# Optimization experiments

Hardware: AMD Instinct MI355X
Metric: run time of the kernel (lower is better)

## Reference

```python
import jax, jax.numpy as jnp
import numpy as np

N, S, D = 4, 2048, 1024
H, HD = 16, 64  # heads, head_dim = patch_size // heads
SCALE = 1.0 / np.float32(np.sqrt(D))  # module divides by sqrt(patch_size), not sqrt(head_dim)


def setup_inputs() -> dict:
    key = jax.random.key(0)
    ks = jax.random.split(key, 8)
    return {
        "values": jax.random.normal(ks[0], (N, S, D), dtype=jnp.float32),
        "keys": jax.random.normal(ks[1], (N, S, D), dtype=jnp.float32),
        "query": jax.random.normal(ks[2], (N, S, D), dtype=jnp.float32),
        "Wv": jax.random.normal(ks[3], (HD, HD), dtype=jnp.float32) / np.float32(np.sqrt(HD)),
        "Wk": jax.random.normal(ks[4], (HD, HD), dtype=jnp.float32) / np.float32(np.sqrt(HD)),
        "Wq": jax.random.normal(ks[5], (HD, HD), dtype=jnp.float32) / np.float32(np.sqrt(HD)),
        "Wo": jax.random.normal(ks[6], (D, D), dtype=jnp.float32) / np.float32(np.sqrt(D)),
        "bo": jnp.zeros((D,), dtype=jnp.float32),
    }


def reference(values, keys, query, Wv, Wk, Wq, Wo, bo):
    n, ql = query.shape[0], query.shape[1]
    # reshape to heads, then per-head shared linear projections (torch Linear: x @ W.T)
    v = jnp.einsum('nlhd,ed->nlhe', values.reshape(n, -1, H, HD), Wv)
    k = jnp.einsum('nkhd,ed->nkhe', keys.reshape(n, -1, H, HD), Wk)
    q = jnp.einsum('nqhd,ed->nqhe', query.reshape(n, -1, H, HD), Wq)
    energy = jnp.einsum('nqhd,nkhd->nhqk', q, k)  # [N,H,Sq,Sk]
    attn = jax.nn.softmax(energy * SCALE, axis=3)
    out = jnp.einsum('nhql,nlhd->nqhd', attn, v).reshape(n, ql, H * HD)
    return out @ Wo.T + bo
```

## Files before the change

### kernel.cpp

```cpp
#include <hip/hip_runtime.h>
#include <stdint.h>

typedef _Float16 f16;
typedef f16 half2_t __attribute__((ext_vector_type(2)));
typedef f16 half4_t __attribute__((ext_vector_type(4)));
typedef f16 half8_t __attribute__((ext_vector_type(8)));
typedef __fp16 fp16x2_t __attribute__((ext_vector_type(2)));
typedef float f32x4 __attribute__((ext_vector_type(4)));

#define N_ 4
#define S_ 2048
#define D_ 1024
#define H_ 16
#define HD_ 64
#define LOG2E 1.44269504088896340736f
#define SCALE_ 0.03125f

typedef __attribute__((address_space(1))) void gvoid;
typedef __attribute__((address_space(3))) void lvoid;

__device__ __forceinline__ void load_lds16(const void* g, void* l) {
  __builtin_amdgcn_global_load_lds((gvoid*)(uintptr_t)g, (lvoid*)l, 16, 0, 0);
}

__device__ __forceinline__ f32x4 mfma32(half8_t a, half8_t b, f32x4 c) {
  return __builtin_amdgcn_mfma_f32_16x16x32_f16(a, b, c, 0, 0, 0);
}

__device__ __forceinline__ half2_t pack_f16(float a, float b) {
  fp16x2_t t = __builtin_amdgcn_cvt_pkrtz(a, b);
  return __builtin_bit_cast(half2_t, t);
}

__global__ void wprep(const float* __restrict__ Wv, const float* __restrict__ Wo,
                      const float* __restrict__ Wq, const float* __restrict__ Wk,
                      const float* __restrict__ V,
                      f16* __restrict__ Wbig, float* __restrict__ Mq,
                      f16* __restrict__ v16) {
  __shared__ char smem[16384];
  int b = blockIdx.x;
  if (b < 1024) {
    int j = b;
#pragma unroll
    for (int c = 0; c < 4; ++c) {
      int i = c * 256 + threadIdx.x;
      int h = i >> 6, dd = i & 63;
      const float* wo = Wo + (size_t)j * 1024 + h * 64;
      float acc = 0.f;
#pragma unroll 8
      for (int e = 0; e < 64; ++e) acc += Wv[e * 64 + dd] * wo[e];
      Wbig[(size_t)j * 1024 + i] = (f16)acc;
    }
  } else if (b < 1040) {
    int tid = (b - 1024) * 256 + threadIdx.x;
    int d = tid >> 6, e = tid & 63;
    float acc = 0.f;
#pragma unroll 8
    for (int r = 0; r < 64; ++r) acc += Wq[r * 64 + d] * Wk[r * 64 + e];
    Mq[d * 64 + e] = acc * (SCALE_ * LOG2E);
  } else {
    f16* lv = (f16*)smem;
    int b2 = b - 1040;
    int n = b2 >> 10, hh = (b2 >> 6) & 15, sb = b2 & 63;
    int t = threadIdx.x;
    {
      int r = t >> 3, ic = t & 7;
      const float* src = V + ((size_t)(n * S_ + sb * 32 + r)) * D_ + hh * HD_ + ic * 8;
      f32x4 a = *(const f32x4*)src;
      f32x4 b3 = *(const f32x4*)(src + 4);
      half8_t hv;
#pragma unroll
      for (int j = 0; j < 4; ++j) { hv[j] = (f16)a[j]; hv[4 + j] = (f16)b3[j]; }
      *(half8_t*)(lv + r * 64 + ic * 8) = hv;
    }
    __syncthreads();
    {
      int mt = t >> 6, L = t & 63;
      int quad = L >> 4, ld = L & 15;
      half8_t o;
#pragma unroll
      for (int j = 0; j < 4; ++j) {
        o[j]     = lv[(quad * 4 + j) * 64 + mt * 16 + ld];
        o[4 + j] = lv[(quad * 4 + j + 16) * 64 + mt * 16 + ld];
      }
      *(half8_t*)(v16 + (((size_t)(n * 16 + hh) * 64 + sb) * 4 + mt) * 512 + L * 8) = o;
    }
  }
}

__global__ __launch_bounds__(256, 3) void prep_qk(const float* __restrict__ Q,
                                                  const float* __restrict__ K,
                                                  const float* __restrict__ Mq,
                                                  f16* __restrict__ q16,
                                                  f16* __restrict__ k16) {
  __shared__ char smem[49152];
  int b = blockIdx.x;
  int hhalf = b & 1;
  int sblk = (b >> 1) & 127;
  int n = b >> 8;
  int t = threadIdx.x;
  int L = t & 63, w = t >> 6;

  const char* Qblk = (const char*)(Q + ((size_t)(n * S_ + sblk * 16)) * D_) + hhalf * 2048;
#pragma unroll
  for (int i = 0; i < 8; ++i) {
    int g = (w * 8 + i) * 64 + L;
    int row = g >> 7, hhg = (g >> 4) & 7, sl = g & 15;
    load_lds16(Qblk + (size_t)row * 4096 + hhg * 256 + ((sl ^ (row & 7)) << 4),
               smem + (w * 8 + i) * 1024);
  }
#pragma unroll
  for (int j = 0; j < 4; ++j)
    load_lds16((const char*)Mq + (size_t)(((w * 4 + j) * 64 + L) << 4),
               smem + 32768 + (w * 4 + j) * 1024);

  const char* Kblk = (const char*)(K + ((size_t)(n * S_ + sblk * 16)) * D_) + hhalf * 2048;
#pragma unroll
  for (int i = 0; i < 4; ++i) {
    int e = i * 256 + t;
    int r = e >> 6, c6 = e & 63;
    const char* src = Kblk + (size_t)r * 4096 + c6 * 32;
    f32x4 a = *(const f32x4*)src;
    f32x4 b2 = *(const f32x4*)(src + 16);
    half8_t hv;
#pragma unroll
    for (int jj = 0; jj < 4; ++jj) { hv[jj] = (f16)a[jj]; hv[4 + jj] = (f16)b2[jj]; }
    int hk = hhalf * 8 + (c6 >> 3), cc = c6 & 7, dp = cc >> 2, qd = cc & 3;
    *(half8_t*)(k16 + ((((size_t)(n * 16 + hk) * 128 + sblk) * 2 + dp) * 512) +
                (qd * 16 + r) * 8) = hv;
  }
  __syncthreads();

  int lq = t & 15, hh8 = (t >> 4) & 7, eh = t >> 7;
  int head = hhalf * 8 + hh8;
  const float* mql = (const float*)(smem + 32768);
  f32x4 acc4[8];
#pragma unroll
  for (int i = 0; i < 8; ++i) acc4[i] = (f32x4){0.f, 0.f, 0.f, 0.f};
  for (int d4 = 0; d4 < 16; ++d4) {
    f32x4 qv = *(const f32x4*)(smem + lq * 2048 + hh8 * 256 + ((d4 ^ (lq & 7)) << 4));
#pragma unroll
    for (int dj = 0; dj < 4; ++dj) {
      const f32x4* mrow = (const f32x4*)(mql + (d4 * 4 + dj) * 64 + eh * 32);
      float qs = qv[dj];
#pragma unroll
      for (int i = 0; i < 8; ++i) acc4[i] += mrow[i] * qs;
    }
  }
  size_t cbase = ((size_t)((n * 16 + head) * 128 + sblk)) * 2;
#pragma unroll
  for (int qd = 0; qd < 4; ++qd) {
    half8_t hv;
    f32x4 a0 = acc4[qd * 2], a1 = acc4[qd * 2 + 1];
#pragma unroll
    for (int jj = 0; jj < 4; ++jj) { hv[jj] = (f16)a0[jj]; hv[4 + jj] = (f16)a1[jj]; }
    *(half8_t*)(q16 + (cbase + eh) * 512 + (qd * 16 + lq) * 8) = hv;
  }
}

__global__ __launch_bounds__(256, 2) void flash(const f16* __restrict__ q16,
                                                const f16* __restrict__ k16,
                                                const f16* __restrict__ v16,
                                                f16* __restrict__ att) {
  int nh = blockIdx.x;
  int qt = blockIdx.y;
  int L = threadIdx.x & 63, w = threadIdx.x >> 6;
  int lq = L & 15, quad = L >> 4;

  const half8_t* qg = (const half8_t*)q16;
  half8_t qB[4][2];
#pragma unroll
  for (int j = 0; j < 4; ++j) {
    size_t qc = ((size_t)(nh * 128 + qt * 16 + w * 4 + j)) * 2;
    qB[j][0] = qg[qc * 64 + L];
    qB[j][1] = qg[(qc + 1) * 64 + L];
  }

  f32x4 accO[4][4];
#pragma unroll
  for (int j = 0; j < 4; ++j)
#pragma unroll
    for (int i = 0; i < 4; ++i) accO[j][i] = (f32x4){0.f, 0.f, 0.f, 0.f};
  f32x4 lvec[4];
#pragma unroll
  for (int j = 0; j < 4; ++j) lvec[j] = (f32x4){0.f, 0.f, 0.f, 0.f};

  const char* kg = (const char*)k16 + (size_t)nh * 262144 + L * 16;
  const char* vg = (const char*)v16 + (size_t)nh * 262144 + L * 16;

  half8_t kfA[4], vfA[4], pb[4];
  f32x4 aQK[2][4];

#define QK16(KF)                                              \
  {                                                           \
    __builtin_amdgcn_s_setprio(1);                            \
    _Pragma("unroll")                                         \
    for (int u = 0; u < 2; ++u) {                             \
      _Pragma("unroll")                                       \
      for (int j = 0; j < 4; ++j) {                           \
        f32x4 a = (f32x4){0.f, 0.f, 0.f, 0.f};                \
        a = mfma32(KF[u * 2], qB[j][0], a);                   \
        a = mfma32(KF[u * 2 + 1], qB[j][1], a);               \
        aQK[u][j] = a;                                        \
      }                                                       \
    }                                                         \
    __builtin_amdgcn_s_setprio(0);                            \
  }

#define PV16(VF)                                              \
  {                                                           \
    __builtin_amdgcn_s_setprio(1);                            \
    _Pragma("unroll")                                         \
    for (int mt2 = 0; mt2 < 4; ++mt2) {                       \
      _Pragma("unroll")                                       \
      for (int j = 0; j < 4; ++j)                             \
        accO[j][mt2] = mfma32(VF[mt2], pb[j], accO[j][mt2]);  \
    }                                                         \
    __builtin_amdgcn_s_setprio(0);                            \
  }

#define EXPPACK                                                             \
  {                                                                         \
    half4_t pc[2][4];                                                       \
    _Pragma("unroll")                                                       \
    for (int u = 0; u < 2; ++u) {                                           \
      _Pragma("unroll")                                                     \
      for (int j = 0; j < 4; ++j) {                                         \
        f32x4 p;                                                            \
        _Pragma("unroll")                                                   \
        for (int r = 0; r < 4; ++r) p[r] = __builtin_amdgcn_exp2f(aQK[u][j][r]); \
        lvec[j] += p;                                                       \
        pc[u][j] = __builtin_shufflevector(pack_f16(p[0], p[1]),            \
                                           pack_f16(p[2], p[3]), 0, 1, 2, 3); \
      }                                                                     \
    }                                                                       \
    _Pragma("unroll")                                                       \
    for (int j = 0; j < 4; ++j)                                             \
      pb[j] = __builtin_shufflevector(pc[0][j], pc[1][j], 0, 1, 2, 3, 4, 5, 6, 7); \
  }

#pragma unroll
  for (int c = 0; c < 4; ++c) {
    kfA[c] = *(const half8_t*)(kg + c * 1024);
    vfA[c] = *(const half8_t*)(vg + c * 1024);
  }
  QK16(kfA);
#pragma unroll
  for (int c = 0; c < 4; ++c) kfA[c] = *(const half8_t*)(kg + 4096 + c * 1024);
  EXPPACK;

  for (int gg = 1; gg < 64; ++gg) {
    QK16(kfA);
    PV16(vfA);
    if (gg + 1 < 64) {
      const char* kb = kg + (size_t)(gg + 1) * 4096;
#pragma unroll
      for (int c = 0; c < 4; ++c) kfA[c] = *(const half8_t*)(kb + c * 1024);
    }
    {
      const char* vb = vg + (size_t)gg * 4096;
#pragma unroll
      for (int c = 0; c < 4; ++c) vfA[c] = *(const half8_t*)(vb + c * 1024);
    }
    EXPPACK;
  }
  PV16(vfA);

#undef QK16
#undef PV16
#undef EXPPACK

  int n = nh >> 4, h = nh & 15;
#pragma unroll
  for (int j = 0; j < 4; ++j) {
    float l = lvec[j][0] + lvec[j][1] + lvec[j][2] + lvec[j][3];
    l += __shfl_xor(l, 16, 64);
    l += __shfl_xor(l, 32, 64);
    float inv_l = 1.0f / l;
    int s = qt * 256 + w * 64 + j * 16 + lq;
    f16* orow = att + ((size_t)(n * S_ + s)) * D_ + h * HD_;
#pragma unroll
    for (int mt2 = 0; mt2 < 4; ++mt2) {
      half4_t o;
#pragma unroll
      for (int r = 0; r < 4; ++r) o[r] = (f16)(accO[j][mt2][r] * inv_l);
      *(half4_t*)(orow + mt2 * 16 + quad * 4) = o;
    }
  }
}

__global__ __launch_bounds__(256, 3) void ogemm(const f16* __restrict__ A, const f16* __restrict__ Bm,
                                                const float* __restrict__ bias, float* __restrict__ C) {
  __shared__ char lds[32768];
  int bm = blockIdx.x, bn = blockIdx.y;
  int L = threadIdx.x & 63, w = threadIdx.x >> 6;
  int wm = w >> 1, wn = w & 1;
  int lq = L & 15, quad = L >> 4;
  int lr = L >> 2, lc = L & 3;
  int src_c = lc ^ (lr & 3);
  f32x4 acc[16];
#pragma unroll
  for (int i = 0; i < 16; ++i) acc[i] = (f32x4){0.f, 0.f, 0.f, 0.f};

  const f16* ga0 = A + ((size_t)(bm * 128 + (w * 2) * 16 + lr)) * 1024 + src_c * 8;
  const f16* gb0 = Bm + ((size_t)(bn * 128 + (w * 2) * 16 + lr)) * 1024 + src_c * 8;

#pragma unroll
  for (int t = 0; t < 2; ++t)
#pragma unroll
    for (int c = 0; c < 2; ++c) {
      load_lds16(ga0 + t * 32 + (size_t)c * 16 * 1024, lds + t * 16384 + (w * 2 + c) * 1024);
      load_lds16(gb0 + t * 32 + (size_t)c * 16 * 1024, lds + t * 16384 + 8192 + (w * 2 + c) * 1024);
    }
  __syncthreads();

  for (int kt = 0; kt < 32; ++kt) {
    const char* base = lds + (kt & 1) * 16384;
    half8_t af[4], bf[4];
#pragma unroll
    for (int t = 0; t < 4; ++t) {
      int ch = quad ^ (lq & 3);
      af[t] = *(const half8_t*)(base + (wm * 64 + t * 16 + lq) * 64 + ch * 16);
      bf[t] = *(const half8_t*)(base + 8192 + (wn * 64 + t * 16 + lq) * 64 + ch * 16);
    }
#pragma unroll
    for (int mt = 0; mt < 4; ++mt)
#pragma unroll
      for (int nt = 0; nt < 4; ++nt)
        acc[mt * 4 + nt] =
            __builtin_amdgcn_mfma_f32_16x16x32_f16(af[mt], bf[nt], acc[mt * 4 + nt], 0, 0, 0);
    __syncthreads();
    if (kt + 2 < 32) {
      char* dst = lds + (kt & 1) * 16384;
#pragma unroll
      for (int c = 0; c < 2; ++c) {
        load_lds16(ga0 + (kt + 2) * 32 + (size_t)c * 16 * 1024, dst + (w * 2 + c) * 1024);
        load_lds16(gb0 + (kt + 2) * 32 + (size_t)c * 16 * 1024, dst + 8192 + (w * 2 + c) * 1024);
      }
    }
  }

#pragma unroll
  for (int nt = 0; nt < 4; ++nt) {
    int col = bn * 128 + wn * 64 + nt * 16 + lq;
    float bv = bias[col];
#pragma unroll
    for (int mt = 0; mt < 4; ++mt) {
#pragma unroll
      for (int r = 0; r < 4; ++r) {
        int row = bm * 128 + wm * 64 + mt * 16 + quad * 4 + r;
        C[(size_t)row * 1024 + col] = acc[mt * 4 + nt][r] + bv;
      }
    }
  }
}

extern "C" void kernel_launch(void* const* d_in, const int* in_sizes, int n_in,
                              void* d_out, int out_size, void* d_ws, size_t ws_size,
                              hipStream_t stream) {
  const float* V  = (const float*)d_in[0];
  const float* K  = (const float*)d_in[1];
  const float* Q  = (const float*)d_in[2];
  const float* Wv = (const float*)d_in[3];
  const float* Wk = (const float*)d_in[4];
  const float* Wq = (const float*)d_in[5];
  const float* Wo = (const float*)d_in[6];
  const float* bo = (const float*)d_in[7];
  float* out = (float*)d_out;

  char* ws = (char*)d_ws;
  float* Mq  = (float*)(ws);
  f16* Wbig  = (f16*)(ws + (1ull << 20));
  f16* q16   = (f16*)(ws + (3ull << 20));
  f16* k16   = (f16*)(ws + (19ull << 20));
  f16* v16   = (f16*)(ws + (35ull << 20));
  f16* att   = (f16*)(ws + (51ull << 20));

  wprep<<<5136, 256, 0, stream>>>(Wv, Wo, Wq, Wk, V, Wbig, Mq, v16);
  prep_qk<<<1024, 256, 0, stream>>>(Q, K, Mq, q16, k16);
  flash<<<dim3(64, 8), 256, 0, stream>>>(q16, k16, v16, att);
  ogemm<<<dim3(64, 8), 256, 0, stream>>>(att, Wbig, bo, out);
}
```

Measured before the change: 263.0 us.

## Stagger odd and even waves' attention loop phases to overlap exp with MFMA

Even and odd waves now run differently ordered software pipelines of the attention inner loop. Odd waves do the exp/pack step before QK and PV, so at any moment one wave of a pair is likely issuing exp (VALU/transcendental) work while the other issues MFMA. The aim is better overlap of these functional units across waves on the same SIMD, in the style of ping-pong scheduling. It duplicates the loop body, which increases code size, and both variants must produce the same results.

New measurement: 268.7 us. 1.02x slower.

```diff
diff --git a/kernel.cpp b/kernel.cpp
--- a/kernel.cpp
+++ b/kernel.cpp
@@ -191,7 +191,7 @@
   half8_t kfA[4], vfA[4], pb[4];
   f32x4 aQK[2][4];
 
-#define QK16(KF)                                              \
+#define QK16                                                  \
   {                                                           \
     __builtin_amdgcn_s_setprio(1);                            \
     _Pragma("unroll")                                         \
@@ -199,24 +199,38 @@
       _Pragma("unroll")                                       \
       for (int j = 0; j < 4; ++j) {                           \
         f32x4 a = (f32x4){0.f, 0.f, 0.f, 0.f};                \
-        a = mfma32(KF[u * 2], qB[j][0], a);                   \
-        a = mfma32(KF[u * 2 + 1], qB[j][1], a);               \
+        a = mfma32(kfA[u * 2], qB[j][0], a);                  \
+        a = mfma32(kfA[u * 2 + 1], qB[j][1], a);              \
         aQK[u][j] = a;                                        \
       }                                                       \
     }                                                         \
     __builtin_amdgcn_s_setprio(0);                            \
   }
 
-#define PV16(VF)                                              \
+#define PV16                                                  \
   {                                                           \
     __builtin_amdgcn_s_setprio(1);                            \
     _Pragma("unroll")                                         \
     for (int mt2 = 0; mt2 < 4; ++mt2) {                       \
       _Pragma("unroll")                                       \
       for (int j = 0; j < 4; ++j)                             \
-        accO[j][mt2] = mfma32(VF[mt2], pb[j], accO[j][mt2]);  \
+        accO[j][mt2] = mfma32(vfA[mt2], pb[j], accO[j][mt2]); \
     }                                                         \
     __builtin_amdgcn_s_setprio(0);                            \
+  }
+
+#define LOADK(GG)                                             \
+  {                                                           \
+    const char* kb_ = kg + (size_t)(GG)*4096;                 \
+    _Pragma("unroll")                                         \
+    for (int c = 0; c < 4; ++c) kfA[c] = *(const half8_t*)(kb_ + c * 1024); \
+  }
+
+#define LOADV(GG)                                             \
+  {                                                           \
+    const char* vb_ = vg + (size_t)(GG)*4096;                 \
+    _Pragma("unroll")                                         \
+    for (int c = 0; c < 4; ++c) vfA[c] = *(const half8_t*)(vb_ + c * 1024); \
   }
 
 #define EXPPACK                                                             \
@@ -239,35 +253,46 @@
       pb[j] = __builtin_shufflevector(pc[0][j], pc[1][j], 0, 1, 2, 3, 4, 5, 6, 7); \
   }
 
-#pragma unroll
-  for (int c = 0; c < 4; ++c) {
-    kfA[c] = *(const half8_t*)(kg + c * 1024);
-    vfA[c] = *(const half8_t*)(vg + c * 1024);
-  }
-  QK16(kfA);
-#pragma unroll
-  for (int c = 0; c < 4; ++c) kfA[c] = *(const half8_t*)(kg + 4096 + c * 1024);
-  EXPPACK;
-
-  for (int gg = 1; gg < 64; ++gg) {
-    QK16(kfA);
-    PV16(vfA);
-    if (gg + 1 < 64) {
-      const char* kb = kg + (size_t)(gg + 1) * 4096;
-#pragma unroll
-      for (int c = 0; c < 4; ++c) kfA[c] = *(const half8_t*)(kb + c * 1024);
-    }
-    {
-      const char* vb = vg + (size_t)gg * 4096;
-#pragma unroll
-      for (int c = 0; c < 4; ++c) vfA[c] = *(const half8_t*)(vb + c * 1024);
-    }
+  if (!(w & 1)) {
+#pragma unroll
+    for (int c = 0; c < 4; ++c) {
+      kfA[c] = *(const half8_t*)(kg + c * 1024);
+      vfA[c] = *(const half8_t*)(vg + c * 1024);
+    }
+    QK16;
+    LOADK(1);
     EXPPACK;
-  }
-  PV16(vfA);
+    for (int gg = 1; gg < 64; ++gg) {
+      QK16;
+      PV16;
+      if (gg + 1 < 64) LOADK(gg + 1);
+      LOADV(gg);
+      EXPPACK;
+    }
+    PV16;
+  } else {
+#pragma unroll
+    for (int c = 0; c < 4; ++c) {
+      kfA[c] = *(const half8_t*)(kg + c * 1024);
+      vfA[c] = *(const half8_t*)(vg + c * 1024);
+    }
+    QK16;
+    LOADK(1);
+    for (int gg = 1; gg < 64; ++gg) {
+      EXPPACK;
+      QK16;
+      if (gg + 1 < 64) LOADK(gg + 1);
+      PV16;
+      LOADV(gg);
+    }
+    EXPPACK;
+    PV16;
+  }
 
 #undef QK16
 #undef PV16
+#undef LOADK
+#undef LOADV
 #undef EXPPACK
 
   int n = nh >> 4, h = nh & 15;
```
